# Optimization experiments

Measured on AMD Instinct MI355X. Metric: run time of the kernel, lower is better.

## Reference

```python
import jax, jax.numpy as jnp
import numpy as np

B = 4        # number of point clouds (equal-sized, batch ids are sorted blocks)
K = 3        # knn_interpolate k
EPS_D = 1e-16
EPS_BN = 1e-5


def setup_inputs() -> dict:
    key = jax.random.key(0)
    ks = jax.random.split(key, 12)
    N_src, N_tgt = 2048, 8192
    C, C_skip = 256, 128
    x = jax.random.normal(ks[0], (B * N_src, C), dtype=jnp.float32)
    pos = jax.random.normal(ks[1], (B * N_src, 3), dtype=jnp.float32)
    x_skip = jax.random.normal(ks[2], (B * N_tgt, C_skip), dtype=jnp.float32)
    pos_skip = jax.random.normal(ks[3], (B * N_tgt, 3), dtype=jnp.float32)
    batch = jnp.repeat(jnp.arange(B, dtype=jnp.int64), N_src)
    batch_skip = jnp.repeat(jnp.arange(B, dtype=jnp.int64), N_tgt)
    d_in = C + C_skip  # 384
    W1 = jax.random.normal(ks[4], (d_in, 256), dtype=jnp.float32) / np.sqrt(d_in)
    b1 = jnp.zeros((256,), dtype=jnp.float32)
    g1 = jnp.ones((256,), dtype=jnp.float32)
    be1 = jnp.zeros((256,), dtype=jnp.float32)
    W2 = jax.random.normal(ks[5], (256, 256), dtype=jnp.float32) / 16.0
    b2 = jnp.zeros((256,), dtype=jnp.float32)
    g2 = jnp.ones((256,), dtype=jnp.float32)
    be2 = jnp.zeros((256,), dtype=jnp.float32)
    return dict(x=x, pos=pos, batch=batch, x_skip=x_skip, pos_skip=pos_skip,
                batch_skip=batch_skip, W1=W1, b1=b1, g1=g1, be1=be1,
                W2=W2, b2=b2, g2=g2, be2=be2)


def _knn_interpolate(x, pos, pos_skip):
    # equal-size clouds: reshape instead of per-batch masking
    C = x.shape[1]
    N = pos.shape[0] // B
    M = pos_skip.shape[0] // B
    ps = pos.reshape(B, N, 3)
    pt = pos_skip.reshape(B, M, 3)
    # squared distances [B, M, N] via |a|^2 + |b|^2 - 2ab
    d2 = (jnp.sum(pt * pt, -1)[:, :, None]
          + jnp.sum(ps * ps, -1)[:, None, :]
          - 2.0 * jnp.einsum('bmd,bnd->bmn', pt, ps))
    neg_d2, idx = jax.lax.top_k(-d2, K)            # idx: [B, M, K]
    w = 1.0 / jnp.maximum(-neg_d2, EPS_D)          # inverse squared distance
    xf = x.reshape(B, N, C)
    feats = xf[jnp.arange(B)[:, None, None], idx]  # [B, M, K, C] irregular gather
    y = jnp.sum(feats * w[..., None], axis=2) / jnp.sum(w, axis=2)[..., None]
    return y.reshape(B * M, C)


def _mlp_block(h, W, b, g, be):
    h = jnp.maximum(h @ W + b, 0.0)                # Linear + ReLU
    mu = jnp.mean(h, axis=0)
    var = jnp.mean((h - mu) ** 2, axis=0)          # biased var (torch BN training)
    return g * (h - mu) / jnp.sqrt(var + EPS_BN) + be


def reference(x, pos, batch, x_skip, pos_skip, batch_skip,
              W1, b1, g1, be1, W2, b2, g2, be2):
    y = _knn_interpolate(x, pos, pos_skip)
    h = jnp.concatenate([y, x_skip], axis=1)       # [B*M, 384]
    h = _mlp_block(h, W1, b1, g1, be1)
    h = _mlp_block(h, W2, b2, g2, be2)
    return h
```

## Files before the change

### kernel.cpp

```cpp
#include <hip/hip_runtime.h>
#include <hip/hip_bf16.h>

typedef __attribute__((ext_vector_type(8))) short short8;
typedef __attribute__((ext_vector_type(4))) float f32x4;

constexpr int BATCH  = 4;
constexpr int NSRC   = 2048;
constexpr int NTGT   = 8192;
constexpr int C_IN   = 256;
constexpr int C_SKIP = 128;
constexpr int DIN    = 384;
constexpr int HID    = 256;
constexpr int MROWS  = BATCH * NTGT;

constexpr int TGT_PER_BLK = 8;
constexpr int KNN_BLOCKS  = MROWS / TGT_PER_BLK;
constexpr int WT_BLOCKS   = 8;
constexpr int LDS_STRIDE  = 36;

__global__ __launch_bounds__(256) void knn_h_kernel(const float* __restrict__ pos,
                                                    const float* __restrict__ pos_skip,
                                                    const float* __restrict__ x,
                                                    const float* __restrict__ xs,
                                                    const float* __restrict__ W1,
                                                    __hip_bfloat16* __restrict__ W1T,
                                                    __hip_bfloat16* __restrict__ H0,
                                                    float* __restrict__ stats) {
    const int blk = blockIdx.x;
    if (blk >= KNN_BLOCKS) {
        const int e = blk - KNN_BLOCKS;
        if (e < WT_BLOCKS) {
            const int r = e * 32 + (threadIdx.x >> 3);
            const int c0 = threadIdx.x & 7;
#pragma unroll
            for (int k = 0; k < DIN / 8; ++k) {
                int c = c0 + k * 8;
                W1T[(size_t)r * DIN + c] = __float2bfloat16(W1[(size_t)c * HID + r]);
            }
        } else {
            for (int i = threadIdx.x; i < 4 * HID; i += 256) stats[i] = 0.0f;
        }
        return;
    }
    __shared__ float4 sp[NSRC];
    __shared__ float  sd[TGT_PER_BLK][3];
    __shared__ int    si[TGT_PER_BLK][3];
    const int t0 = blk * TGT_PER_BLK;
    const int b  = t0 / NTGT;
    const float* ps = pos + (size_t)b * NSRC * 3;
    for (int j = threadIdx.x; j < NSRC; j += 256) {
        float X = ps[j * 3 + 0], Y = ps[j * 3 + 1], Z = ps[j * 3 + 2];
        float s2 = __fadd_rn(__fadd_rn(__fmul_rn(X, X), __fmul_rn(Y, Y)), __fmul_rn(Z, Z));
        sp[j] = make_float4(X, Y, Z, s2);
    }
    __syncthreads();
    const int g  = threadIdx.x >> 5;
    const int s  = threadIdx.x & 31;
    const int tr = t0 + g;
    const float px = pos_skip[tr * 3 + 0], py = pos_skip[tr * 3 + 1], pz = pos_skip[tr * 3 + 2];
    const float pt2 = __fadd_rn(__fadd_rn(__fmul_rn(px, px), __fmul_rn(py, py)), __fmul_rn(pz, pz));
    float bd0 = 3e38f, bd1 = 3e38f, bd2 = 3e38f;
    int   bi0 = 0x7fffffff, bi1 = 0x7fffffff, bi2 = 0x7fffffff;
#pragma unroll 8
    for (int k = 0; k < NSRC / 32; ++k) {
        const int j = k * 32 + s;
        float4 sv = sp[j];
        float dot = __fadd_rn(__fadd_rn(__fmul_rn(px, sv.x), __fmul_rn(py, sv.y)), __fmul_rn(pz, sv.z));
        float d2  = __fsub_rn(__fadd_rn(pt2, sv.w), __fmul_rn(2.0f, dot));
        bool c0 = d2 < bd0, c1 = d2 < bd1, c2 = d2 < bd2;
        bd2 = c1 ? bd1 : (c2 ? d2 : bd2);  bi2 = c1 ? bi1 : (c2 ? j : bi2);
        bd1 = c0 ? bd0 : (c1 ? d2 : bd1);  bi1 = c0 ? bi0 : (c1 ? j : bi1);
        bd0 = c0 ? d2  : bd0;              bi0 = c0 ? j  : bi0;
    }
#pragma unroll
    for (int m = 1; m <= 16; m <<= 1) {
        float od0 = __shfl_xor(bd0, m), od1 = __shfl_xor(bd1, m), od2 = __shfl_xor(bd2, m);
        int   oi0 = __shfl_xor(bi0, m), oi1 = __shfl_xor(bi1, m), oi2 = __shfl_xor(bi2, m);
#pragma unroll
        for (int e = 0; e < 3; ++e) {
            float d = e == 0 ? od0 : (e == 1 ? od1 : od2);
            int   i = e == 0 ? oi0 : (e == 1 ? oi1 : oi2);
            bool c0 = (d < bd0) || (d == bd0 && i < bi0);
            bool c1 = (d < bd1) || (d == bd1 && i < bi1);
            bool c2 = (d < bd2) || (d == bd2 && i < bi2);
            bd2 = c1 ? bd1 : (c2 ? d : bd2);  bi2 = c1 ? bi1 : (c2 ? i : bi2);
            bd1 = c0 ? bd0 : (c1 ? d : bd1);  bi1 = c0 ? bi0 : (c1 ? i : bi1);
            bd0 = c0 ? d   : bd0;             bi0 = c0 ? i  : bi0;
        }
    }
    if (s == 0) {
        sd[g][0] = bd0; sd[g][1] = bd1; sd[g][2] = bd2;
        si[g][0] = bi0; si[g][1] = bi1; si[g][2] = bi2;
    }
    __syncthreads();
    const int w = threadIdx.x >> 6, lane = threadIdx.x & 63;
    const float* xb = x + (size_t)b * NSRC * C_IN;
#pragma unroll
    for (int u = 0; u < 2; ++u) {
        const int tt = w * 2 + u;
        const int r  = t0 + tt;
        float w0 = 1.0f / fmaxf(sd[tt][0], 1e-16f);
        float w1 = 1.0f / fmaxf(sd[tt][1], 1e-16f);
        float w2 = 1.0f / fmaxf(sd[tt][2], 1e-16f);
        float inv = 1.0f / ((w0 + w1) + w2);
        const float* f0 = xb + (size_t)si[tt][0] * C_IN;
        const float* f1 = xb + (size_t)si[tt][1] * C_IN;
        const float* f2 = xb + (size_t)si[tt][2] * C_IN;
        __hip_bfloat16* o = H0 + (size_t)r * DIN;
#pragma unroll
        for (int kk = 0; kk < 4; ++kk) {
            int c = lane + kk * 64;
            float v = ((w0 * f0[c] + w1 * f1[c]) + w2 * f2[c]) * inv;
            o[c] = __float2bfloat16(v);
        }
        const float* srow = xs + (size_t)r * C_SKIP;
#pragma unroll
        for (int kk = 0; kk < 2; ++kk) {
            int c = lane + kk * 64;
            o[C_IN + c] = __float2bfloat16(srow[c]);
        }
    }
}

template <int K, bool OUT_BF16>
__global__ __launch_bounds__(256, 2) void gemm_kernel(const __hip_bfloat16* __restrict__ A,
                                                      const __hip_bfloat16* __restrict__ WT,
                                                      const float* __restrict__ bias,
                                                      void* __restrict__ outp,
                                                      float* __restrict__ colsum,
                                                      float* __restrict__ colsq) {
    __shared__ short As[128 * LDS_STRIDE];
    const int t = threadIdx.x;
    const int m0 = blockIdx.x * 128, n0 = blockIdx.y * 128;
    const int wid = t >> 6, lane = t & 63;
    const int wr = wid >> 1, wc = wid & 1;
    const int l15 = lane & 15, l4 = lane >> 4;
    const int arow = t >> 1, acol8 = (t & 1) * 8;
    f32x4 acc[4][4] = {};
    const short* Ash = (const short*)A;
    const short* Wsh = (const short*)WT;
    for (int kt = 0; kt < K / 32; ++kt) {
        short8 v0 = *(const short8*)(Ash + (size_t)(m0 + arow) * K + kt * 32 + acol8);
        short8 v1 = *(const short8*)(Ash + (size_t)(m0 + arow) * K + kt * 32 + acol8 + 16);
        __syncthreads();
        *(short8*)(&As[arow * LDS_STRIDE + acol8]) = v0;
        *(short8*)(&As[arow * LDS_STRIDE + acol8 + 16]) = v1;
        __syncthreads();
        short8 af[4], bfr[4];
#pragma unroll
        for (int mi = 0; mi < 4; ++mi)
            af[mi] = *(const short8*)(&As[(wr * 64 + mi * 16 + l15) * LDS_STRIDE + l4 * 8]);
#pragma unroll
        for (int ni = 0; ni < 4; ++ni)
            bfr[ni] = *(const short8*)(Wsh + (size_t)(n0 + wc * 64 + ni * 16 + l15) * K + kt * 32 + l4 * 8);
#pragma unroll
        for (int mi = 0; mi < 4; ++mi)
#pragma unroll
            for (int ni = 0; ni < 4; ++ni)
                acc[mi][ni] = __builtin_amdgcn_mfma_f32_16x16x32_bf16(af[mi], bfr[ni], acc[mi][ni], 0, 0, 0);
    }
    float bv[4];
    int col[4];
#pragma unroll
    for (int ni = 0; ni < 4; ++ni) {
        col[ni] = n0 + wc * 64 + ni * 16 + l15;
        bv[ni] = bias[col[ni]];
    }
    float csum[4] = {0, 0, 0, 0}, csq[4] = {0, 0, 0, 0};
    __hip_bfloat16* ob = (__hip_bfloat16*)outp;
    float* of = (float*)outp;
#pragma unroll
    for (int mi = 0; mi < 4; ++mi) {
#pragma unroll
        for (int r = 0; r < 4; ++r) {
            int rowg = m0 + wr * 64 + mi * 16 + l4 * 4 + r;
#pragma unroll
            for (int ni = 0; ni < 4; ++ni) {
                float v = fmaxf(acc[mi][ni][r] + bv[ni], 0.0f);
                if (OUT_BF16) ob[(size_t)rowg * HID + col[ni]] = __float2bfloat16(v);
                else          of[(size_t)rowg * HID + col[ni]] = v;
                csum[ni] += v;
                csq[ni] += v * v;
            }
        }
    }
#pragma unroll
    for (int ni = 0; ni < 4; ++ni) {
        float sv = csum[ni], q = csq[ni];
        sv += __shfl_xor(sv, 16); sv += __shfl_xor(sv, 32);
        q  += __shfl_xor(q, 16);  q  += __shfl_xor(q, 32);
        if (l4 == 0) {
            atomicAdd(&colsum[col[ni]], sv);
            atomicAdd(&colsq[col[ni]], q);
        }
    }
}

__global__ void finalize_kernel(const float* __restrict__ sum, const float* __restrict__ sq,
                                const float* __restrict__ g, const float* __restrict__ be,
                                float* __restrict__ scale, float* __restrict__ shift) {
    int c = threadIdx.x;
    float mu  = sum[c] * (1.0f / MROWS);
    float var = sq[c] * (1.0f / MROWS) - mu * mu;
    float inv = 1.0f / sqrtf(var + 1e-5f);
    float sc = g[c] * inv;
    scale[c] = sc;
    shift[c] = be[c] - mu * sc;
}

__global__ __launch_bounds__(256) void foldw2_kernel(const float* __restrict__ W2,
                                                     const float* __restrict__ b2,
                                                     const float* __restrict__ sum1,
                                                     const float* __restrict__ sq1,
                                                     const float* __restrict__ g1,
                                                     const float* __restrict__ be1,
                                                     __hip_bfloat16* __restrict__ W2T,
                                                     float* __restrict__ bias2f) {
    __shared__ float red[256];
    const int n = blockIdx.x, k = threadIdx.x;
    float mu  = sum1[k] * (1.0f / MROWS);
    float var = sq1[k] * (1.0f / MROWS) - mu * mu;
    float scv = g1[k] / sqrtf(var + 1e-5f);
    float shv = be1[k] - mu * scv;
    float v = W2[(size_t)k * HID + n];
    W2T[(size_t)n * HID + k] = __float2bfloat16(scv * v);
    red[k] = shv * v;
    __syncthreads();
    for (int s = 128; s > 0; s >>= 1) {
        if (k < s) red[k] += red[k + s];
        __syncthreads();
    }
    if (k == 0) bias2f[n] = b2[n] + red[0];
}

__global__ __launch_bounds__(256) void bn2_kernel(float* __restrict__ out,
                                                  const float* __restrict__ scale2,
                                                  const float* __restrict__ shift2) {
    int idx = blockIdx.x * blockDim.x + threadIdx.x;
    const int total = MROWS * HID / 4;
    for (; idx < total; idx += gridDim.x * blockDim.x) {
        float4 v = ((float4*)out)[idx];
        int c = (idx * 4) & (HID - 1);
        float4 sc = *(const float4*)(scale2 + c);
        float4 sh = *(const float4*)(shift2 + c);
        v.x = sc.x * v.x + sh.x;
        v.y = sc.y * v.y + sh.y;
        v.z = sc.z * v.z + sh.z;
        v.w = sc.w * v.w + sh.w;
        ((float4*)out)[idx] = v;
    }
}

extern "C" void kernel_launch(void* const* d_in, const int* in_sizes, int n_in,
                              void* d_out, int out_size, void* d_ws, size_t ws_size,
                              hipStream_t stream) {
    const float* x    = (const float*)d_in[0];
    const float* pos  = (const float*)d_in[1];
    const float* xs   = (const float*)d_in[3];
    const float* poss = (const float*)d_in[4];
    const float* W1   = (const float*)d_in[6];
    const float* b1   = (const float*)d_in[7];
    const float* g1   = (const float*)d_in[8];
    const float* be1  = (const float*)d_in[9];
    const float* W2   = (const float*)d_in[10];
    const float* b2   = (const float*)d_in[11];
    const float* g2   = (const float*)d_in[12];
    const float* be2  = (const float*)d_in[13];

    char* ws = (char*)d_ws;
    size_t off = 0;
    auto alloc = [&](size_t bytes) -> void* {
        void* p = ws + off;
        off += (bytes + 255) & ~(size_t)255;
        return p;
    };
    __hip_bfloat16* W1T   = (__hip_bfloat16*)alloc((size_t)HID * DIN * 2);
    __hip_bfloat16* W2T   = (__hip_bfloat16*)alloc((size_t)HID * HID * 2);
    float*          stats = (float*)alloc(4 * HID * sizeof(float));
    float *sum1 = stats, *sq1 = stats + HID, *sum2 = stats + 2 * HID, *sq2 = stats + 3 * HID;
    float* sc = (float*)alloc(3 * HID * sizeof(float));
    float *scale2 = sc, *shift2 = sc + HID, *bias2f = sc + 2 * HID;
    __hip_bfloat16* H0 = (__hip_bfloat16*)alloc((size_t)MROWS * DIN * 2);
    __hip_bfloat16* H1 = (__hip_bfloat16*)alloc((size_t)MROWS * HID * 2);

    knn_h_kernel<<<KNN_BLOCKS + WT_BLOCKS + 1, 256, 0, stream>>>(pos, poss, x, xs, W1, W1T, H0, stats);
    gemm_kernel<DIN, true><<<dim3(MROWS / 128, 2), 256, 0, stream>>>(H0, W1T, b1, H1, sum1, sq1);
    foldw2_kernel<<<HID, 256, 0, stream>>>(W2, b2, sum1, sq1, g1, be1, W2T, bias2f);
    gemm_kernel<HID, false><<<dim3(MROWS / 128, 2), 256, 0, stream>>>(H1, W2T, bias2f, d_out, sum2, sq2);
    finalize_kernel<<<1, 256, 0, stream>>>(sum2, sq2, g2, be2, scale2, shift2);
    bn2_kernel<<<2048, 256, 0, stream>>>((float*)d_out, scale2, shift2);
}
```

Baseline: 144.7 us.

## Widen KNN blocks, pack distance math, full-width GEMM tiles, bf16 H2 with fused BN2

The KNN kernel now runs 512 threads per block handling 16 targets, and computes two candidate distances per iteration with packed float2 arithmetic. Contraction is disabled so the distances keep the same rounding as before. The GEMM now computes all 256 output columns per block, so each A tile is loaded once instead of twice. The second GEMM writes a bf16 intermediate instead of fp32, and the separate finalize kernel is folded into the BN2 kernel, which now reads bf16 and writes fp32. This removes a launch and halves the intermediate traffic, at the cost of more registers per GEMM block, lower occupancy, and bf16 rounding before the second batch norm.

```diff
diff --git a/kernel.cpp b/kernel.cpp
--- a/kernel.cpp
+++ b/kernel.cpp
@@ -3,6 +3,8 @@
 
 typedef __attribute__((ext_vector_type(8))) short short8;
 typedef __attribute__((ext_vector_type(4))) float f32x4;
+typedef __attribute__((ext_vector_type(2))) float f32x2;
+typedef __attribute__((ext_vector_type(8))) float f32x8;
 
 constexpr int BATCH  = 4;
 constexpr int NSRC   = 2048;
@@ -13,32 +15,33 @@
 constexpr int HID    = 256;
 constexpr int MROWS  = BATCH * NTGT;
 
-constexpr int TGT_PER_BLK = 8;
+constexpr int TGT_PER_BLK = 16;
 constexpr int KNN_BLOCKS  = MROWS / TGT_PER_BLK;
 constexpr int WT_BLOCKS   = 8;
 constexpr int LDS_STRIDE  = 36;
 
-__global__ __launch_bounds__(256) void knn_h_kernel(const float* __restrict__ pos,
-                                                    const float* __restrict__ pos_skip,
-                                                    const float* __restrict__ x,
-                                                    const float* __restrict__ xs,
-                                                    const float* __restrict__ W1,
-                                                    __hip_bfloat16* __restrict__ W1T,
-                                                    __hip_bfloat16* __restrict__ H0,
-                                                    float* __restrict__ stats) {
+__global__ __launch_bounds__(512, 4) void knn_h_kernel(const float* __restrict__ pos,
+                                                       const float* __restrict__ pos_skip,
+                                                       const float* __restrict__ x,
+                                                       const float* __restrict__ xs,
+                                                       const float* __restrict__ W1,
+                                                       __hip_bfloat16* __restrict__ W1T,
+                                                       __hip_bfloat16* __restrict__ H0,
+                                                       float* __restrict__ stats) {
+#pragma clang fp contract(off)
     const int blk = blockIdx.x;
     if (blk >= KNN_BLOCKS) {
         const int e = blk - KNN_BLOCKS;
         if (e < WT_BLOCKS) {
-            const int r = e * 32 + (threadIdx.x >> 3);
-            const int c0 = threadIdx.x & 7;
-#pragma unroll
-            for (int k = 0; k < DIN / 8; ++k) {
-                int c = c0 + k * 8;
+            const int r  = e * 32 + (threadIdx.x >> 4);
+            const int c0 = threadIdx.x & 15;
+#pragma unroll
+            for (int k = 0; k < DIN / 16; ++k) {
+                int c = c0 + k * 16;
                 W1T[(size_t)r * DIN + c] = __float2bfloat16(W1[(size_t)c * HID + r]);
             }
         } else {
-            for (int i = threadIdx.x; i < 4 * HID; i += 256) stats[i] = 0.0f;
+            for (int i = threadIdx.x; i < 4 * HID; i += 512) stats[i] = 0.0f;
         }
         return;
     }
@@ -48,9 +51,9 @@
     const int t0 = blk * TGT_PER_BLK;
     const int b  = t0 / NTGT;
     const float* ps = pos + (size_t)b * NSRC * 3;
-    for (int j = threadIdx.x; j < NSRC; j += 256) {
+    for (int j = threadIdx.x; j < NSRC; j += 512) {
         float X = ps[j * 3 + 0], Y = ps[j * 3 + 1], Z = ps[j * 3 + 2];
-        float s2 = __fadd_rn(__fadd_rn(__fmul_rn(X, X), __fmul_rn(Y, Y)), __fmul_rn(Z, Z));
+        float s2 = ((X * X) + (Y * Y)) + (Z * Z);
         sp[j] = make_float4(X, Y, Z, s2);
     }
     __syncthreads();
@@ -58,19 +61,28 @@
     const int s  = threadIdx.x & 31;
     const int tr = t0 + g;
     const float px = pos_skip[tr * 3 + 0], py = pos_skip[tr * 3 + 1], pz = pos_skip[tr * 3 + 2];
-    const float pt2 = __fadd_rn(__fadd_rn(__fmul_rn(px, px), __fmul_rn(py, py)), __fmul_rn(pz, pz));
+    const float pt2 = ((px * px) + (py * py)) + (pz * pz);
+    const f32x2 px2 = {px, px}, py2 = {py, py}, pz2 = {pz, pz}, ptv = {pt2, pt2};
     float bd0 = 3e38f, bd1 = 3e38f, bd2 = 3e38f;
     int   bi0 = 0x7fffffff, bi1 = 0x7fffffff, bi2 = 0x7fffffff;
-#pragma unroll 8
-    for (int k = 0; k < NSRC / 32; ++k) {
-        const int j = k * 32 + s;
-        float4 sv = sp[j];
-        float dot = __fadd_rn(__fadd_rn(__fmul_rn(px, sv.x), __fmul_rn(py, sv.y)), __fmul_rn(pz, sv.z));
-        float d2  = __fsub_rn(__fadd_rn(pt2, sv.w), __fmul_rn(2.0f, dot));
-        bool c0 = d2 < bd0, c1 = d2 < bd1, c2 = d2 < bd2;
-        bd2 = c1 ? bd1 : (c2 ? d2 : bd2);  bi2 = c1 ? bi1 : (c2 ? j : bi2);
-        bd1 = c0 ? bd0 : (c1 ? d2 : bd1);  bi1 = c0 ? bi0 : (c1 ? j : bi1);
-        bd0 = c0 ? d2  : bd0;              bi0 = c0 ? j  : bi0;
+#pragma unroll 4
+    for (int k = 0; k < NSRC / 64; ++k) {
+        const int j1 = k * 64 + s;
+        const int j2 = j1 + 32;
+        float4 sa = sp[j1];
+        float4 sb = sp[j2];
+        f32x2 vx = {sa.x, sb.x}, vy = {sa.y, sb.y}, vz = {sa.z, sb.z}, vw = {sa.w, sb.w};
+        f32x2 dot = ((px2 * vx) + (py2 * vy)) + (pz2 * vz);
+        f32x2 d2v = (ptv + vw) - (f32x2{2.0f, 2.0f} * dot);
+#pragma unroll
+        for (int h = 0; h < 2; ++h) {
+            float d2 = h == 0 ? d2v.x : d2v.y;
+            int   j  = h == 0 ? j1 : j2;
+            bool c0 = d2 < bd0, c1 = d2 < bd1, c2 = d2 < bd2;
+            bd2 = c1 ? bd1 : (c2 ? d2 : bd2);  bi2 = c1 ? bi1 : (c2 ? j : bi2);
+            bd1 = c0 ? bd0 : (c1 ? d2 : bd1);  bi1 = c0 ? bi0 : (c1 ? j : bi1);
+            bd0 = c0 ? d2  : bd0;              bi0 = c0 ? j  : bi0;
+        }
     }
 #pragma unroll
     for (int m = 1; m <= 16; m <<= 1) {
@@ -122,21 +134,21 @@
     }
 }
 
-template <int K, bool OUT_BF16>
-__global__ __launch_bounds__(256, 2) void gemm_kernel(const __hip_bfloat16* __restrict__ A,
+template <int K>
+__global__ __launch_bounds__(256, 1) void gemm_kernel(const __hip_bfloat16* __restrict__ A,
                                                       const __hip_bfloat16* __restrict__ WT,
                                                       const float* __restrict__ bias,
-                                                      void* __restrict__ outp,
+                                                      __hip_bfloat16* __restrict__ outp,
                                                       float* __restrict__ colsum,
                                                       float* __restrict__ colsq) {
     __shared__ short As[128 * LDS_STRIDE];
     const int t = threadIdx.x;
-    const int m0 = blockIdx.x * 128, n0 = blockIdx.y * 128;
+    const int m0 = blockIdx.x * 128;
     const int wid = t >> 6, lane = t & 63;
-    const int wr = wid >> 1, wc = wid & 1;
+    const int wr = wid & 1, wcq = wid >> 1;
     const int l15 = lane & 15, l4 = lane >> 4;
     const int arow = t >> 1, acol8 = (t & 1) * 8;
-    f32x4 acc[4][4] = {};
+    f32x4 acc[4][8] = {};
     const short* Ash = (const short*)A;
     const short* Wsh = (const short*)WT;
     for (int kt = 0; kt < K / 32; ++kt) {
@@ -146,46 +158,43 @@
         *(short8*)(&As[arow * LDS_STRIDE + acol8]) = v0;
         *(short8*)(&As[arow * LDS_STRIDE + acol8 + 16]) = v1;
         __syncthreads();
-        short8 af[4], bfr[4];
+        short8 af[4], bfr[8];
 #pragma unroll
         for (int mi = 0; mi < 4; ++mi)
             af[mi] = *(const short8*)(&As[(wr * 64 + mi * 16 + l15) * LDS_STRIDE + l4 * 8]);
 #pragma unroll
-        for (int ni = 0; ni < 4; ++ni)
-            bfr[ni] = *(const short8*)(Wsh + (size_t)(n0 + wc * 64 + ni * 16 + l15) * K + kt * 32 + l4 * 8);
+        for (int ni = 0; ni < 8; ++ni)
+            bfr[ni] = *(const short8*)(Wsh + (size_t)(wcq * 128 + ni * 16 + l15) * K + kt * 32 + l4 * 8);
 #pragma unroll
         for (int mi = 0; mi < 4; ++mi)
 #pragma unroll
-            for (int ni = 0; ni < 4; ++ni)
+            for (int ni = 0; ni < 8; ++ni)
                 acc[mi][ni] = __builtin_amdgcn_mfma_f32_16x16x32_bf16(af[mi], bfr[ni], acc[mi][ni], 0, 0, 0);
     }
-    float bv[4];
-    int col[4];
-#pragma unroll
-    for (int ni = 0; ni < 4; ++ni) {
-        col[ni] = n0 + wc * 64 + ni * 16 + l15;
+    float bv[8];
+    int col[8];
+#pragma unroll
+    for (int ni = 0; ni < 8; ++ni) {
+        col[ni] = wcq * 128 + ni * 16 + l15;
         bv[ni] = bias[col[ni]];
     }
-    float csum[4] = {0, 0, 0, 0}, csq[4] = {0, 0, 0, 0};
-    __hip_bfloat16* ob = (__hip_bfloat16*)outp;
-    float* of = (float*)outp;
+    float csum[8] = {}, csq[8] = {};
 #pragma unroll
     for (int mi = 0; mi < 4; ++mi) {
 #pragma unroll
         for (int r = 0; r < 4; ++r) {
             int rowg = m0 + wr * 64 + mi * 16 + l4 * 4 + r;
 #pragma unroll
-            for (int ni = 0; ni < 4; ++ni) {
+            for (int ni = 0; ni < 8; ++ni) {
                 float v = fmaxf(acc[mi][ni][r] + bv[ni], 0.0f);
-                if (OUT_BF16) ob[(size_t)rowg * HID + col[ni]] = __float2bfloat16(v);
-                else          of[(size_t)rowg * HID + col[ni]] = v;
+                outp[(size_t)rowg * HID + col[ni]] = __float2bfloat16(v);
                 csum[ni] += v;
                 csq[ni] += v * v;
             }
         }
     }
 #pragma unroll
-    for (int ni = 0; ni < 4; ++ni) {
+    for (int ni = 0; ni < 8; ++ni) {
         float sv = csum[ni], q = csq[ni];
         sv += __shfl_xor(sv, 16); sv += __shfl_xor(sv, 32);
         q  += __shfl_xor(q, 16);  q  += __shfl_xor(q, 32);
@@ -194,18 +203,6 @@
             atomicAdd(&colsq[col[ni]], q);
         }
     }
-}
-
-__global__ void finalize_kernel(const float* __restrict__ sum, const float* __restrict__ sq,
-                                const float* __restrict__ g, const float* __restrict__ be,
-                                float* __restrict__ scale, float* __restrict__ shift) {
-    int c = threadIdx.x;
-    float mu  = sum[c] * (1.0f / MROWS);
-    float var = sq[c] * (1.0f / MROWS) - mu * mu;
-    float inv = 1.0f / sqrtf(var + 1e-5f);
-    float sc = g[c] * inv;
-    scale[c] = sc;
-    shift[c] = be[c] - mu * sc;
 }
 
 __global__ __launch_bounds__(256) void foldw2_kernel(const float* __restrict__ W2,
@@ -233,21 +230,34 @@
     if (k == 0) bias2f[n] = b2[n] + red[0];
 }
 
-__global__ __launch_bounds__(256) void bn2_kernel(float* __restrict__ out,
-                                                  const float* __restrict__ scale2,
-                                                  const float* __restrict__ shift2) {
+__global__ __launch_bounds__(256) void bn2_kernel(const __hip_bfloat16* __restrict__ h2,
+                                                  const float* __restrict__ sum2,
+                                                  const float* __restrict__ sq2,
+                                                  const float* __restrict__ g2,
+                                                  const float* __restrict__ be2,
+                                                  float* __restrict__ out) {
+    __shared__ float lsc[HID], lsh[HID];
+    {
+        int c = threadIdx.x;
+        float mu  = sum2[c] * (1.0f / MROWS);
+        float var = sq2[c] * (1.0f / MROWS) - mu * mu;
+        float scv = g2[c] / sqrtf(var + 1e-5f);
+        lsc[c] = scv;
+        lsh[c] = be2[c] - mu * scv;
+    }
+    __syncthreads();
     int idx = blockIdx.x * blockDim.x + threadIdx.x;
-    const int total = MROWS * HID / 4;
+    const int total = MROWS * HID / 8;
     for (; idx < total; idx += gridDim.x * blockDim.x) {
-        float4 v = ((float4*)out)[idx];
-        int c = (idx * 4) & (HID - 1);
-        float4 sc = *(const float4*)(scale2 + c);
-        float4 sh = *(const float4*)(shift2 + c);
-        v.x = sc.x * v.x + sh.x;
-        v.y = sc.y * v.y + sh.y;
-        v.z = sc.z * v.z + sh.z;
-        v.w = sc.w * v.w + sh.w;
-        ((float4*)out)[idx] = v;
+        short8 v = *(const short8*)(h2 + (size_t)idx * 8);
+        int c = (idx * 8) & (HID - 1);
+        f32x8 o;
+#pragma unroll
+        for (int e = 0; e < 8; ++e) {
+            float f = __uint_as_float(((unsigned)(unsigned short)v[e]) << 16);
+            o[e] = lsc[c + e] * f + lsh[c + e];
+        }
+        *(f32x8*)(out + (size_t)idx * 8) = o;
     }
 }
 
@@ -278,15 +288,14 @@
     __hip_bfloat16* W2T   = (__hip_bfloat16*)alloc((size_t)HID * HID * 2);
     float*          stats = (float*)alloc(4 * HID * sizeof(float));
     float *sum1 = stats, *sq1 = stats + HID, *sum2 = stats + 2 * HID, *sq2 = stats + 3 * HID;
-    float* sc = (float*)alloc(3 * HID * sizeof(float));
-    float *scale2 = sc, *shift2 = sc + HID, *bias2f = sc + 2 * HID;
+    float*          bias2f = (float*)alloc(HID * sizeof(float));
     __hip_bfloat16* H0 = (__hip_bfloat16*)alloc((size_t)MROWS * DIN * 2);
     __hip_bfloat16* H1 = (__hip_bfloat16*)alloc((size_t)MROWS * HID * 2);
-
-    knn_h_kernel<<<KNN_BLOCKS + WT_BLOCKS + 1, 256, 0, stream>>>(pos, poss, x, xs, W1, W1T, H0, stats);
-    gemm_kernel<DIN, true><<<dim3(MROWS / 128, 2), 256, 0, stream>>>(H0, W1T, b1, H1, sum1, sq1);
+    __hip_bfloat16* H2 = H0;
+
+    knn_h_kernel<<<KNN_BLOCKS + WT_BLOCKS + 1, 512, 0, stream>>>(pos, poss, x, xs, W1, W1T, H0, stats);
+    gemm_kernel<DIN><<<MROWS / 128, 256, 0, stream>>>(H0, W1T, b1, H1, sum1, sq1);
     foldw2_kernel<<<HID, 256, 0, stream>>>(W2, b2, sum1, sq1, g1, be1, W2T, bias2f);
-    gemm_kernel<HID, false><<<dim3(MROWS / 128, 2), 256, 0, stream>>>(H1, W2T, bias2f, d_out, sum2, sq2);
-    finalize_kernel<<<1, 256, 0, stream>>>(sum2, sq2, g2, be2, scale2, shift2);
-    bn2_kernel<<<2048, 256, 0, stream>>>((float*)d_out, scale2, shift2);
-}
+    gemm_kernel<HID><<<MROWS / 128, 256, 0, stream>>>(H1, W2T, bias2f, H2, sum2, sq2);
+    bn2_kernel<<<1024, 256, 0, stream>>>(H2, sum2, sq2, g2, be2, (float*)d_out);
+}
```

Measured after the change: 136.8 us. 5.4% less time.
